# Performance work log

Hardware: AMD Instinct MI355X
Metric: run time of the kernel (lower is better)

## Reference

```python
import jax, jax.numpy as jnp
import numpy as np

REGIONS = [(0, 16), (17, 21), (22, 26), (27, 30), (31, 35), (36, 41), (42, 47), (48, 59), (60, 67)]
LN_EPS = 1e-5


def setup_inputs() -> dict:
    key = jax.random.key(0)
    ks = jax.random.split(key, 8)
    B, T, N, D = 32, 128, 68, 128
    sc = 1.0 / np.sqrt(D)
    inp = {
        "lm_data": jax.random.normal(ks[0], (B, T, N, D), jnp.float32),
        "adj": jax.random.uniform(ks[1], (77, 77), jnp.float32) / 77.0,
        "Wr": jax.random.normal(ks[2], (D, 1), jnp.float32) * sc,
        "br": jnp.zeros((1,), jnp.float32),
        "W0": jax.random.normal(ks[3], (D, D), jnp.float32) * sc,
        "b0": jnp.zeros((D,), jnp.float32),
        "W1": jax.random.normal(ks[4], (D, D), jnp.float32) * sc,
        "b1": jnp.zeros((D,), jnp.float32),
        "W2": jax.random.normal(ks[5], (D, D), jnp.float32) * sc,
        "b2": jnp.zeros((D,), jnp.float32),
        "W3": jax.random.normal(ks[6], (D, D), jnp.float32) * sc,
        "b3": jnp.zeros((D,), jnp.float32),
        "gamma": jnp.ones((D,), jnp.float32),
        "beta": jnp.zeros((D,), jnp.float32),
    }
    return inp


def _region_pool(x, Wr, br):
    # x: [B,T,R,D] -> attention-pooled [B,T,D]
    scores = jnp.einsum('btrd,do->btro', x, Wr) + br  # [B,T,R,1]
    w = jax.nn.softmax(scores, axis=-2)
    return jnp.sum(w * x, axis=-2)


def reference(lm_data, adj, Wr, br, W0, b0, W1, b1, W2, b2, W3, b3, gamma, beta):
    # init_global_nodes: gather each region, attention-pool, scatter into 9 global nodes
    global_nodes = jnp.stack(
        [_region_pool(lm_data[..., s:e + 1, :], Wr, br) for s, e in REGIONS], axis=2
    )  # [B,T,9,D]
    x = jnp.concatenate([lm_data, global_nodes], axis=2)  # [B,T,77,D]

    # 4-layer residual GCN: relu(Linear(adj @ x))
    layers = [(W0, b0), (W1, b1), (W2, b2), (W3, b3)]
    residual = x
    for i, (W, b) in enumerate(layers):
        agg = jnp.einsum('nm,btmd->btnd', adj, x)
        out = jax.nn.relu(agg @ W + b)
        if i < len(layers) - 1:
            out = out + residual  # feature dims all equal
            residual = out
        x = out

    # LayerNorm (dropout is identity at eval)
    mu = jnp.mean(x, axis=-1, keepdims=True)
    var = jnp.var(x, axis=-1, keepdims=True)
    x = (x - mu) / jnp.sqrt(var + LN_EPS) * gamma + beta
    return x
```

## Files before the change

kernel.cpp:

```cpp
#include <hip/hip_runtime.h>
#include <stdint.h>

typedef __attribute__((ext_vector_type(8))) short bf16x8;
typedef __attribute__((ext_vector_type(4))) float f32x4;
typedef unsigned short u16;
typedef __attribute__((ext_vector_type(4))) unsigned short us4;
typedef __attribute__((ext_vector_type(8))) unsigned short us8;

#define NP 104
#define FPD 136

__device__ __constant__ int c_RS[9] = {0, 17, 22, 27, 31, 36, 42, 48, 60};
__device__ __constant__ int c_RE[9] = {16, 21, 26, 30, 35, 41, 47, 59, 67};

__device__ __forceinline__ float b2f(u16 h) {
    union { unsigned int u; float f; } v;
    v.u = ((unsigned int)h) << 16;
    return v.f;
}
__device__ __forceinline__ u16 f2b(float f) {
    union { float f; unsigned int u; } v;
    v.f = f;
    unsigned int r = v.u + 0x7fffu + ((v.u >> 16) & 1u);
    return (u16)(r >> 16);
}

__global__ void prep_kernel(const float* __restrict__ adj,
                            const float* __restrict__ W0, const float* __restrict__ W1,
                            const float* __restrict__ W2, const float* __restrict__ W3,
                            u16* __restrict__ adjp, u16* __restrict__ WT) {
    int id = blockIdx.x * 256 + threadIdx.x;
    if (id < 80 * 96) {
        int m = id / 96, k = id - m * 96;
        adjp[id] = (m < 77 && k < 77) ? f2b(adj[m * 77 + k]) : (u16)0;
    }
    {
        int l = id >> 14, r = id & 16383;
        int n = r >> 7, k = r & 127;
        const float* W = (l == 0) ? W0 : (l == 1) ? W1 : (l == 2) ? W2 : W3;
        WT[id] = f2b(W[k * 128 + n]);
    }
}

__global__ __launch_bounds__(256, 2) void gcn_kernel(
    const float* __restrict__ lm, const float* __restrict__ Wr,
    const float* __restrict__ b0, const float* __restrict__ b1,
    const float* __restrict__ b2, const float* __restrict__ b3,
    const float* __restrict__ gamma, const float* __restrict__ beta,
    const u16* __restrict__ adjp, const u16* __restrict__ WT,
    float* __restrict__ out) {
    __shared__ __align__(16) u16 xT[128 * NP];
    __shared__ __align__(16) u16 ag[80 * FPD];
    __shared__ float WrF[128];
    __shared__ float biasF[512];
    __shared__ float gamF[128], betF[128];
    __shared__ float scoreS[80], wtS[80], muS[80], rsS[80];

    const int t = threadIdx.x;
    const int lane = t & 63;
    const int w = t >> 6;
    const int lo = lane & 15;
    const int qd = lane >> 4;
    const size_t pos = blockIdx.x;
    const float* lmp = lm + pos * (68 * 128);

    if (t < 128) {
        WrF[t] = Wr[t];
        gamF[t] = gamma[t];
        betF[t] = beta[t];
        biasF[t] = b0[t];
        biasF[128 + t] = b1[t];
        biasF[256 + t] = b2[t];
        biasF[384 + t] = b3[t];
    }
    for (int i = t; i < 128 * NP / 8; i += 256) ((uint4*)xT)[i] = make_uint4(0, 0, 0, 0);
    const float4* lmp4 = (const float4*)lmp;
    for (int c = t; c < 68 * 32; c += 256) {
        int n = c >> 5, q = c & 31;
        float4 v = lmp4[c];
        us4 o;
        o[0] = f2b(v.x); o[1] = f2b(v.y); o[2] = f2b(v.z); o[3] = f2b(v.w);
        *(us4*)(&ag[n * FPD + q * 4]) = o;
    }
    __syncthreads();

    for (int c = t; c < 68 * 16; c += 256) {
        int d8 = c / 68, n = c - d8 * 68;
        us8 v = *(const us8*)(&ag[n * FPD + d8 * 8]);
#pragma unroll
        for (int j = 0; j < 8; j++) xT[(d8 * 8 + j) * NP + n] = v[j];
    }
    if (t < 68) {
        float s = 0.f;
        for (int d8 = 0; d8 < 16; d8++) {
            us8 v = *(const us8*)(&ag[t * FPD + d8 * 8]);
#pragma unroll
            for (int j = 0; j < 8; j++) s += b2f(v[j]) * WrF[d8 * 8 + j];
        }
        scoreS[t] = s;
    }
    __syncthreads();

    if (t < 9) {
        int s0 = c_RS[t], e0 = c_RE[t];
        float mx = -3e38f;
        for (int i = s0; i <= e0; i++) mx = fmaxf(mx, scoreS[i]);
        float sum = 0.f;
        for (int i = s0; i <= e0; i++) sum += __expf(scoreS[i] - mx);
        float inv = 1.f / sum;
        for (int i = s0; i <= e0; i++) wtS[i] = __expf(scoreS[i] - mx) * inv;
    }
    __syncthreads();

    for (int c = t; c < 9 * 128; c += 256) {
        int r = c >> 7, d = c & 127;
        int s0 = c_RS[r], e0 = c_RE[r];
        float g = 0.f;
        for (int n = s0; n <= e0; n++) g += wtS[n] * b2f(ag[n * FPD + d]);
        xT[d * NP + 68 + r] = f2b(g);
    }
    __syncthreads();

    for (int l = 0; l < 4; l++) {
        f32x4 acc[5][2];
#pragma unroll
        for (int a = 0; a < 5; a++)
#pragma unroll
            for (int j = 0; j < 2; j++)
#pragma unroll
                for (int r = 0; r < 4; r++) acc[a][j][r] = 0.f;
#pragma unroll
        for (int ks = 0; ks < 3; ks++) {
            bf16x8 bA[5], bB[2];
#pragma unroll
            for (int tm = 0; tm < 5; tm++)
                bA[tm] = *(const bf16x8*)(adjp + (tm * 16 + lo) * 96 + ks * 32 + qd * 8);
#pragma unroll
            for (int j = 0; j < 2; j++) {
                int tn = w + 4 * j;
                bB[j] = *(const bf16x8*)(&xT[(tn * 16 + lo) * NP + ks * 32 + qd * 8]);
            }
#pragma unroll
            for (int tm = 0; tm < 5; tm++)
#pragma unroll
                for (int j = 0; j < 2; j++)
                    acc[tm][j] = __builtin_amdgcn_mfma_f32_16x16x32_bf16(bA[tm], bB[j], acc[tm][j], 0, 0, 0);
        }
#pragma unroll
        for (int tm = 0; tm < 5; tm++)
#pragma unroll
            for (int j = 0; j < 2; j++) {
                int col = (w + 4 * j) * 16 + lo;
#pragma unroll
                for (int r = 0; r < 4; r++) {
                    int row = tm * 16 + qd * 4 + r;
                    ag[row * FPD + col] = f2b(acc[tm][j][r]);
                }
            }
        __syncthreads();

#pragma unroll
        for (int a = 0; a < 5; a++)
#pragma unroll
            for (int j = 0; j < 2; j++)
#pragma unroll
                for (int r = 0; r < 4; r++) acc[a][j][r] = 0.f;
        const u16* WTl = WT + l * 16384;
#pragma unroll
        for (int ks = 0; ks < 4; ks++) {
            bf16x8 aF[5], bW[2];
#pragma unroll
            for (int tm = 0; tm < 5; tm++)
                aF[tm] = *(const bf16x8*)(&ag[(tm * 16 + lo) * FPD + ks * 32 + qd * 8]);
#pragma unroll
            for (int j = 0; j < 2; j++) {
                int tn = w + 4 * j;
                bW[j] = *(const bf16x8*)(WTl + (tn * 16 + lo) * 128 + ks * 32 + qd * 8);
            }
#pragma unroll
            for (int tm = 0; tm < 5; tm++)
#pragma unroll
                for (int j = 0; j < 2; j++)
                    acc[tm][j] = __builtin_amdgcn_mfma_f32_16x16x32_bf16(aF[tm], bW[j], acc[tm][j], 0, 0, 0);
        }
        if (l == 3) __syncthreads();
#pragma unroll
        for (int j = 0; j < 2; j++) {
            int col = (w + 4 * j) * 16 + lo;
            float bv = biasF[l * 128 + col];
#pragma unroll
            for (int tm = 0; tm < 5; tm++)
#pragma unroll
                for (int r = 0; r < 4; r++) {
                    int row = tm * 16 + qd * 4 + r;
                    float v = fmaxf(acc[tm][j][r] + bv, 0.f);
                    if (l < 3) {
                        v += b2f(xT[col * NP + row]);
                        xT[col * NP + row] = f2b(v);
                    } else {
                        ag[row * FPD + col] = f2b(v);
                    }
                }
        }
        __syncthreads();
    }

    if (t < 77) {
        float s = 0.f, ss = 0.f;
        for (int d = 0; d < 128; d += 2) {
            uint32_t v = *(const uint32_t*)(&ag[t * FPD + d]);
            float a = b2f((u16)(v & 0xffff)), b = b2f((u16)(v >> 16));
            s += a + b;
            ss += a * a + b * b;
        }
        float mu = s * (1.f / 128.f);
        float var = ss * (1.f / 128.f) - mu * mu;
        muS[t] = mu;
        rsS[t] = rsqrtf(var + 1e-5f);
    }
    __syncthreads();

    float* outp = out + pos * 9856;
    for (int c = t; c < 77 * 32; c += 256) {
        int n = c >> 5, q = c & 31;
        us4 v = *(const us4*)(&ag[n * FPD + q * 4]);
        float mu = muS[n], rs = rsS[n];
        float4 o;
        int d = q * 4;
        o.x = (b2f(v[0]) - mu) * rs * gamF[d + 0] + betF[d + 0];
        o.y = (b2f(v[1]) - mu) * rs * gamF[d + 1] + betF[d + 1];
        o.z = (b2f(v[2]) - mu) * rs * gamF[d + 2] + betF[d + 2];
        o.w = (b2f(v[3]) - mu) * rs * gamF[d + 3] + betF[d + 3];
        *(float4*)(outp + n * 128 + d) = o;
    }
}

extern "C" void kernel_launch(void* const* d_in, const int* in_sizes, int n_in,
                              void* d_out, int out_size, void* d_ws, size_t ws_size,
                              hipStream_t stream) {
    const float* lm = (const float*)d_in[0];
    const float* adj = (const float*)d_in[1];
    const float* Wr = (const float*)d_in[2];
    const float* W0 = (const float*)d_in[4];
    const float* b0 = (const float*)d_in[5];
    const float* W1 = (const float*)d_in[6];
    const float* b1 = (const float*)d_in[7];
    const float* W2 = (const float*)d_in[8];
    const float* b2 = (const float*)d_in[9];
    const float* W3 = (const float*)d_in[10];
    const float* b3 = (const float*)d_in[11];
    const float* gamma = (const float*)d_in[12];
    const float* beta = (const float*)d_in[13];

    u16* adjp = (u16*)d_ws;
    u16* WT = (u16*)((char*)d_ws + 80 * 96 * 2);

    prep_kernel<<<256, 256, 0, stream>>>(adj, W0, W1, W2, W3, adjp, WT);
    gcn_kernel<<<4096, 256, 0, stream>>>(lm, Wr, b0, b1, b2, b3, gamma, beta,
                                         adjp, WT, (float*)d_out);
}
```

Measured before the change: 508.3 us.

## Shrink LDS footprint with swizzled layout to raise occupancy to four blocks

Cuts the per-block shared memory by replacing the padded row layouts with an unpadded 128-wide buffer that uses XOR swizzling to avoid bank conflicts. It shrinks the transposed buffer to 80 columns by remapping the adjacency K padding, and drops the scratch arrays for bias, gamma and beta, reading those from global memory instead. The softmax is merged into the pooling loop, LayerNorm statistics are split across two threads, and the residual update is vectorised. Launch bounds now request 4 blocks per CU, which limits registers per thread and risks spills.

```diff
diff --git a/kernel.cpp b/kernel.cpp
--- a/kernel.cpp
+++ b/kernel.cpp
@@ -7,8 +7,7 @@
 typedef __attribute__((ext_vector_type(4))) unsigned short us4;
 typedef __attribute__((ext_vector_type(8))) unsigned short us8;
 
-#define NP 104
-#define FPD 136
+#define NP 80
 
 __device__ __constant__ int c_RS[9] = {0, 17, 22, 27, 31, 36, 42, 48, 60};
 __device__ __constant__ int c_RE[9] = {16, 21, 26, 30, 35, 41, 47, 59, 67};
@@ -23,6 +22,9 @@
     v.f = f;
     unsigned int r = v.u + 0x7fffu + ((v.u >> 16) & 1u);
     return (u16)(r >> 16);
+}
+__device__ __forceinline__ int agx(int row, int col) {
+    return row * 128 + (col ^ (((row & 4) << 3) | ((row & 8) << 1)));
 }
 
 __global__ void prep_kernel(const float* __restrict__ adj,
@@ -31,8 +33,14 @@
                             u16* __restrict__ adjp, u16* __restrict__ WT) {
     int id = blockIdx.x * 256 + threadIdx.x;
     if (id < 80 * 96) {
-        int m = id / 96, k = id - m * 96;
-        adjp[id] = (m < 77 && k < 77) ? f2b(adj[m * 77 + k]) : (u16)0;
+        int m = id / 96, c = id - m * 96;
+        float v = 0.f;
+        if (m < 77) {
+            int k = (c < 64) ? c : (c - 16);
+            if (c >= 64 && c < 80) k = 77;
+            if (k < 77) v = adj[m * 77 + k];
+        }
+        adjp[id] = f2b(v);
     }
     {
         int l = id >> 14, r = id & 16383;
@@ -42,7 +50,7 @@
     }
 }
 
-__global__ __launch_bounds__(256, 2) void gcn_kernel(
+__global__ __launch_bounds__(256, 4) void gcn_kernel(
     const float* __restrict__ lm, const float* __restrict__ Wr,
     const float* __restrict__ b0, const float* __restrict__ b1,
     const float* __restrict__ b2, const float* __restrict__ b3,
@@ -50,11 +58,7 @@
     const u16* __restrict__ adjp, const u16* __restrict__ WT,
     float* __restrict__ out) {
     __shared__ __align__(16) u16 xT[128 * NP];
-    __shared__ __align__(16) u16 ag[80 * FPD];
-    __shared__ float WrF[128];
-    __shared__ float biasF[512];
-    __shared__ float gamF[128], betF[128];
-    __shared__ float scoreS[80], wtS[80], muS[80], rsS[80];
+    __shared__ __align__(16) u16 ag[80 * 128];
 
     const int t = threadIdx.x;
     const int lane = t & 63;
@@ -64,60 +68,54 @@
     const size_t pos = blockIdx.x;
     const float* lmp = lm + pos * (68 * 128);
 
+    float* WrF = (float*)&ag[68 * 128];
+    float* scoreS = (float*)&ag[70 * 128];
+    float* muP = (float*)xT;
+    float* rsP = muP + 80;
+
     if (t < 128) {
         WrF[t] = Wr[t];
-        gamF[t] = gamma[t];
-        betF[t] = beta[t];
-        biasF[t] = b0[t];
-        biasF[128 + t] = b1[t];
-        biasF[256 + t] = b2[t];
-        biasF[384 + t] = b3[t];
-    }
-    for (int i = t; i < 128 * NP / 8; i += 256) ((uint4*)xT)[i] = make_uint4(0, 0, 0, 0);
+        xT[t * NP + 77] = 0; xT[t * NP + 78] = 0; xT[t * NP + 79] = 0;
+    }
     const float4* lmp4 = (const float4*)lmp;
     for (int c = t; c < 68 * 32; c += 256) {
         int n = c >> 5, q = c & 31;
         float4 v = lmp4[c];
         us4 o;
         o[0] = f2b(v.x); o[1] = f2b(v.y); o[2] = f2b(v.z); o[3] = f2b(v.w);
-        *(us4*)(&ag[n * FPD + q * 4]) = o;
+        *(us4*)(&ag[agx(n, q * 4)]) = o;
     }
     __syncthreads();
 
     for (int c = t; c < 68 * 16; c += 256) {
         int d8 = c / 68, n = c - d8 * 68;
-        us8 v = *(const us8*)(&ag[n * FPD + d8 * 8]);
+        us8 v = *(const us8*)(&ag[agx(n, d8 * 8)]);
 #pragma unroll
         for (int j = 0; j < 8; j++) xT[(d8 * 8 + j) * NP + n] = v[j];
     }
     if (t < 68) {
         float s = 0.f;
         for (int d8 = 0; d8 < 16; d8++) {
-            us8 v = *(const us8*)(&ag[t * FPD + d8 * 8]);
+            us8 v = *(const us8*)(&ag[agx(t, d8 * 8)]);
 #pragma unroll
             for (int j = 0; j < 8; j++) s += b2f(v[j]) * WrF[d8 * 8 + j];
         }
         scoreS[t] = s;
-    }
-    __syncthreads();
-
-    if (t < 9) {
-        int s0 = c_RS[t], e0 = c_RE[t];
-        float mx = -3e38f;
-        for (int i = s0; i <= e0; i++) mx = fmaxf(mx, scoreS[i]);
-        float sum = 0.f;
-        for (int i = s0; i <= e0; i++) sum += __expf(scoreS[i] - mx);
-        float inv = 1.f / sum;
-        for (int i = s0; i <= e0; i++) wtS[i] = __expf(scoreS[i] - mx) * inv;
     }
     __syncthreads();
 
     for (int c = t; c < 9 * 128; c += 256) {
         int r = c >> 7, d = c & 127;
         int s0 = c_RS[r], e0 = c_RE[r];
-        float g = 0.f;
-        for (int n = s0; n <= e0; n++) g += wtS[n] * b2f(ag[n * FPD + d]);
-        xT[d * NP + 68 + r] = f2b(g);
+        float mx = -3e38f;
+        for (int i = s0; i <= e0; i++) mx = fmaxf(mx, scoreS[i]);
+        float sum = 0.f, g = 0.f;
+        for (int i = s0; i <= e0; i++) {
+            float e = __expf(scoreS[i] - mx);
+            sum += e;
+            g += e * b2f(ag[agx(i, d)]);
+        }
+        xT[d * NP + 68 + r] = f2b(g / sum);
     }
     __syncthreads();
 
@@ -131,15 +129,14 @@
                 for (int r = 0; r < 4; r++) acc[a][j][r] = 0.f;
 #pragma unroll
         for (int ks = 0; ks < 3; ks++) {
+            const int koff = (ks == 2) ? 48 : ks * 32;
             bf16x8 bA[5], bB[2];
 #pragma unroll
             for (int tm = 0; tm < 5; tm++)
                 bA[tm] = *(const bf16x8*)(adjp + (tm * 16 + lo) * 96 + ks * 32 + qd * 8);
 #pragma unroll
-            for (int j = 0; j < 2; j++) {
-                int tn = w + 4 * j;
-                bB[j] = *(const bf16x8*)(&xT[(tn * 16 + lo) * NP + ks * 32 + qd * 8]);
-            }
+            for (int j = 0; j < 2; j++)
+                bB[j] = *(const bf16x8*)(&xT[((w + 4 * j) * 16 + lo) * NP + koff + qd * 8]);
 #pragma unroll
             for (int tm = 0; tm < 5; tm++)
 #pragma unroll
@@ -152,10 +149,8 @@
             for (int j = 0; j < 2; j++) {
                 int col = (w + 4 * j) * 16 + lo;
 #pragma unroll
-                for (int r = 0; r < 4; r++) {
-                    int row = tm * 16 + qd * 4 + r;
-                    ag[row * FPD + col] = f2b(acc[tm][j][r]);
-                }
+                for (int r = 0; r < 4; r++)
+                    ag[agx(tm * 16 + qd * 4 + r, col)] = f2b(acc[tm][j][r]);
             }
         __syncthreads();
 
@@ -171,67 +166,78 @@
             bf16x8 aF[5], bW[2];
 #pragma unroll
             for (int tm = 0; tm < 5; tm++)
-                aF[tm] = *(const bf16x8*)(&ag[(tm * 16 + lo) * FPD + ks * 32 + qd * 8]);
-#pragma unroll
-            for (int j = 0; j < 2; j++) {
-                int tn = w + 4 * j;
-                bW[j] = *(const bf16x8*)(WTl + (tn * 16 + lo) * 128 + ks * 32 + qd * 8);
-            }
+                aF[tm] = *(const bf16x8*)(&ag[agx(tm * 16 + lo, ks * 32 + qd * 8)]);
+#pragma unroll
+            for (int j = 0; j < 2; j++)
+                bW[j] = *(const bf16x8*)(WTl + ((w + 4 * j) * 16 + lo) * 128 + ks * 32 + qd * 8);
 #pragma unroll
             for (int tm = 0; tm < 5; tm++)
 #pragma unroll
                 for (int j = 0; j < 2; j++)
                     acc[tm][j] = __builtin_amdgcn_mfma_f32_16x16x32_bf16(aF[tm], bW[j], acc[tm][j], 0, 0, 0);
         }
+        const float* bl = (l == 0) ? b0 : (l == 1) ? b1 : (l == 2) ? b2 : b3;
         if (l == 3) __syncthreads();
 #pragma unroll
         for (int j = 0; j < 2; j++) {
             int col = (w + 4 * j) * 16 + lo;
-            float bv = biasF[l * 128 + col];
-#pragma unroll
-            for (int tm = 0; tm < 5; tm++)
-#pragma unroll
-                for (int r = 0; r < 4; r++) {
-                    int row = tm * 16 + qd * 4 + r;
-                    float v = fmaxf(acc[tm][j][r] + bv, 0.f);
-                    if (l < 3) {
-                        v += b2f(xT[col * NP + row]);
-                        xT[col * NP + row] = f2b(v);
-                    } else {
-                        ag[row * FPD + col] = f2b(v);
+            float bv = bl[col];
+            if (l < 3) {
+#pragma unroll
+                for (int tm = 0; tm < 5; tm++) {
+                    int nb = tm * 16 + qd * 4;
+                    us4 old4 = *(const us4*)(&xT[col * NP + nb]);
+                    us4 nv;
+#pragma unroll
+                    for (int r = 0; r < 4; r++) {
+                        float v = fmaxf(acc[tm][j][r] + bv, 0.f) + b2f(old4[r]);
+                        nv[r] = f2b(v);
                     }
+                    *(us4*)(&xT[col * NP + nb]) = nv;
                 }
+            } else {
+#pragma unroll
+                for (int tm = 0; tm < 5; tm++)
+#pragma unroll
+                    for (int r = 0; r < 4; r++)
+                        ag[agx(tm * 16 + qd * 4 + r, col)] = f2b(fmaxf(acc[tm][j][r] + bv, 0.f));
+            }
         }
         __syncthreads();
     }
 
-    if (t < 77) {
+    if (t < 154) {
+        int n = t >> 1, h = t & 1;
         float s = 0.f, ss = 0.f;
-        for (int d = 0; d < 128; d += 2) {
-            uint32_t v = *(const uint32_t*)(&ag[t * FPD + d]);
-            float a = b2f((u16)(v & 0xffff)), b = b2f((u16)(v >> 16));
-            s += a + b;
-            ss += a * a + b * b;
-        }
-        float mu = s * (1.f / 128.f);
-        float var = ss * (1.f / 128.f) - mu * mu;
-        muS[t] = mu;
-        rsS[t] = rsqrtf(var + 1e-5f);
+#pragma unroll
+        for (int i = 0; i < 8; i++) {
+            us8 v = *(const us8*)(&ag[agx(n, h * 64 + i * 8)]);
+#pragma unroll
+            for (int j = 0; j < 8; j++) { float a = b2f(v[j]); s += a; ss += a * a; }
+        }
+        s += __shfl_xor(s, 1);
+        ss += __shfl_xor(ss, 1);
+        if (h == 0) {
+            float mu = s * (1.f / 128.f);
+            muP[n] = mu;
+            rsP[n] = rsqrtf(ss * (1.f / 128.f) - mu * mu + 1e-5f);
+        }
     }
     __syncthreads();
 
     float* outp = out + pos * 9856;
     for (int c = t; c < 77 * 32; c += 256) {
         int n = c >> 5, q = c & 31;
-        us4 v = *(const us4*)(&ag[n * FPD + q * 4]);
-        float mu = muS[n], rs = rsS[n];
+        us4 v = *(const us4*)(&ag[agx(n, q * 4)]);
+        float mu = muP[n], rs = rsP[n];
+        float4 gm = *(const float4*)(gamma + q * 4);
+        float4 bt = *(const float4*)(beta + q * 4);
         float4 o;
-        int d = q * 4;
-        o.x = (b2f(v[0]) - mu) * rs * gamF[d + 0] + betF[d + 0];
-        o.y = (b2f(v[1]) - mu) * rs * gamF[d + 1] + betF[d + 1];
-        o.z = (b2f(v[2]) - mu) * rs * gamF[d + 2] + betF[d + 2];
-        o.w = (b2f(v[3]) - mu) * rs * gamF[d + 3] + betF[d + 3];
-        *(float4*)(outp + n * 128 + d) = o;
+        o.x = (b2f(v[0]) - mu) * rs * gm.x + bt.x;
+        o.y = (b2f(v[1]) - mu) * rs * gm.y + bt.y;
+        o.z = (b2f(v[2]) - mu) * rs * gm.z + bt.z;
+        o.w = (b2f(v[3]) - mu) * rs * gm.w + bt.w;
+        *(float4*)(outp + n * 128 + q * 4) = o;
     }
 }
 
```

Result: faster. 467.6 us (-8.0%).
